# Kernel tuning notes

Measured on AMD Instinct MI355X. Metric: run time of the kernel, lower is better.

Reference implementation:

```python
import jax, jax.numpy as jnp
import numpy as np
import math

D_MODEL = 512
NHEAD = 8
HEAD = D_MODEL // NHEAD


def _pe(length, d):
    pos = np.arange(length)[:, None].astype(np.float32)
    div = np.exp(np.arange(0, d, 2).astype(np.float32) * (-math.log(10000.0) / d))
    pe = np.zeros((length, d), np.float32)
    pe[:, 0::2] = np.sin(pos * div)
    pe[:, 1::2] = np.cos(pos * div)
    return jnp.asarray(pe)


def _ln(x, g, b, eps=1e-5):
    m = x.mean(-1, keepdims=True)
    v = ((x - m) ** 2).mean(-1, keepdims=True)
    return (x - m) / jnp.sqrt(v + eps) * g + b


def _mha(q_in, k_in, v_in, w_in, b_in, w_out, b_out, mask=None):
    d = q_in.shape[-1]
    wq, wk, wv = jnp.split(w_in, 3, axis=0)
    bq, bk, bv = jnp.split(b_in, 3, axis=0)
    B, Sq, _ = q_in.shape
    Sk = k_in.shape[1]
    q = (q_in @ wq.T + bq).reshape(B, Sq, NHEAD, HEAD)
    k = (k_in @ wk.T + bk).reshape(B, Sk, NHEAD, HEAD)
    v = (v_in @ wv.T + bv).reshape(B, Sk, NHEAD, HEAD)
    s = jnp.einsum('bqhd,bkhd->bhqk', q, k) / math.sqrt(HEAD)
    if mask is not None:
        s = s + mask
    a = jax.nn.softmax(s, axis=-1)
    o = jnp.einsum('bhqk,bkhd->bqhd', a, v).reshape(B, Sq, d)
    return o @ w_out.T + b_out


def setup_inputs() -> dict:
    rng = np.random.default_rng(0)
    def r(*s):
        return jnp.asarray(rng.standard_normal(s, dtype=np.float32) * 0.02)
    L, d, ff, di, do = 6, 512, 2048, 64, 64
    B, S, T = 4, 512, 256
    return dict(
        src=jnp.asarray(rng.standard_normal((B, S, di), dtype=np.float32)),
        tgt=jnp.asarray(rng.standard_normal((B, T, do), dtype=np.float32)),
        enc_in_w=r(d, di), enc_in_b=r(d),
        dec_in_w=r(d, do), dec_in_b=r(d),
        out_w=r(do, d), out_b=r(do),
        enc_attn_w=r(L, 3 * d, d), enc_attn_b=r(L, 3 * d),
        enc_out_w=r(L, d, d), enc_out_b=r(L, d),
        enc_ff1_w=r(L, ff, d), enc_ff1_b=r(L, ff),
        enc_ff2_w=r(L, d, ff), enc_ff2_b=r(L, d),
        enc_ln1_g=jnp.ones((L, d)), enc_ln1_b=jnp.zeros((L, d)),
        enc_ln2_g=jnp.ones((L, d)), enc_ln2_b=jnp.zeros((L, d)),
        dec_sa_w=r(L, 3 * d, d), dec_sa_b=r(L, 3 * d),
        dec_sa_out_w=r(L, d, d), dec_sa_out_b=r(L, d),
        dec_ca_w=r(L, 3 * d, d), dec_ca_b=r(L, 3 * d),
        dec_ca_out_w=r(L, d, d), dec_ca_out_b=r(L, d),
        dec_ff1_w=r(L, ff, d), dec_ff1_b=r(L, ff),
        dec_ff2_w=r(L, d, ff), dec_ff2_b=r(L, d),
        dec_ln1_g=jnp.ones((L, d)), dec_ln1_b=jnp.zeros((L, d)),
        dec_ln2_g=jnp.ones((L, d)), dec_ln2_b=jnp.zeros((L, d)),
        dec_ln3_g=jnp.ones((L, d)), dec_ln3_b=jnp.zeros((L, d)),
    )


def reference(src, tgt, enc_in_w, enc_in_b, dec_in_w, dec_in_b, out_w, out_b,
              enc_attn_w, enc_attn_b, enc_out_w, enc_out_b,
              enc_ff1_w, enc_ff1_b, enc_ff2_w, enc_ff2_b,
              enc_ln1_g, enc_ln1_b, enc_ln2_g, enc_ln2_b,
              dec_sa_w, dec_sa_b, dec_sa_out_w, dec_sa_out_b,
              dec_ca_w, dec_ca_b, dec_ca_out_w, dec_ca_out_b,
              dec_ff1_w, dec_ff1_b, dec_ff2_w, dec_ff2_b,
              dec_ln1_g, dec_ln1_b, dec_ln2_g, dec_ln2_b, dec_ln3_g, dec_ln3_b):
    d = D_MODEL
    sq = math.sqrt(d)
    S, T = src.shape[1], tgt.shape[1]
    L = enc_attn_w.shape[0]
    # encoder: 'cosine' pos encoding (dropout disabled / eval)
    x = (src @ enc_in_w.T + enc_in_b) * sq + _pe(S, d)[None]
    for i in range(L):
        a = _mha(x, x, x, enc_attn_w[i], enc_attn_b[i], enc_out_w[i], enc_out_b[i])
        x = _ln(x + a, enc_ln1_g[i], enc_ln1_b[i])
        f = jax.nn.relu(x @ enc_ff1_w[i].T + enc_ff1_b[i]) @ enc_ff2_w[i].T + enc_ff2_b[i]
        x = _ln(x + f, enc_ln2_g[i], enc_ln2_b[i])
    memory = x
    # decoder: teacher-forced prefix loop == single causal-masked pass.
    # NOTE: original adds pe[0] to EVERY step (pos_encoder on a length-1 slice).
    y = (tgt @ dec_in_w.T + dec_in_b) * sq + _pe(1, d)[0]
    mask = jnp.where(jnp.tril(jnp.ones((T, T), bool)), 0.0, -1e9).astype(y.dtype)
    for i in range(L):
        a = _mha(y, y, y, dec_sa_w[i], dec_sa_b[i], dec_sa_out_w[i], dec_sa_out_b[i], mask)
        y = _ln(y + a, dec_ln1_g[i], dec_ln1_b[i])
        c = _mha(y, memory, memory, dec_ca_w[i], dec_ca_b[i], dec_ca_out_w[i], dec_ca_out_b[i])
        y = _ln(y + c, dec_ln2_g[i], dec_ln2_b[i])
        f = jax.nn.relu(y @ dec_ff1_w[i].T + dec_ff1_b[i]) @ dec_ff2_w[i].T + dec_ff2_b[i]
        y = _ln(y + f, dec_ln3_g[i], dec_ln3_b[i])
    return y @ out_w.T + out_b
```

## Files before the change

kernel.cpp:

```cpp
#include <hip/hip_runtime.h>
#include <hip/hip_bf16.h>
#include <math.h>

#define BB 4
#define SEQ 512
#define TGT 256
#define DM 512
#define FFD 2048
#define NH 8
#define HD 64
#define NL 6

typedef unsigned short u16;
typedef __attribute__((ext_vector_type(4))) float f4;
typedef __attribute__((ext_vector_type(4))) unsigned short us4;
typedef __attribute__((ext_vector_type(8))) unsigned short us8;
typedef __attribute__((ext_vector_type(8))) short s8;

__device__ inline u16 f2b(float f) {
    __hip_bfloat16 h = __float2bfloat16(f);
    return *reinterpret_cast<u16*>(&h);
}
__device__ inline float b2f(u16 u) {
    unsigned int x = ((unsigned int)u) << 16;
    float f;
    __builtin_memcpy(&f, &x, 4);
    return f;
}
__device__ inline us4 cvt4(f4 v) {
    us4 u;
    u.x = f2b(v.x); u.y = f2b(v.y); u.z = f2b(v.z); u.w = f2b(v.w);
    return u;
}

__global__ __launch_bounds__(256) void cast4_k(const float* __restrict__ in,
                                               u16* __restrict__ out, int n4)
{
    int i = blockIdx.x * blockDim.x + threadIdx.x;
    if (i < n4) ((us4*)out)[i] = cvt4(((const f4*)in)[i]);
}

template <int RELU, int OUTF32, int BM>
__global__ __launch_bounds__(256) void mgemm_k(
    const u16* __restrict__ A, const u16* __restrict__ W,
    const float* __restrict__ bias, const u16* __restrict__ resid,
    void* __restrict__ Cv, int M, int N, int K, float alpha)
{
    constexpr int MI = BM / 32;
    __shared__ u16 As[2][BM][72];
    __shared__ u16 Bs[2][64][72];
    const int bm = blockIdx.y * BM, bn = blockIdx.x * 64;
    const int tid = threadIdx.x;
    const int wave = tid >> 6, lane = tid & 63;
    const int wr = (wave >> 1) * (BM / 2), wc = (wave & 1) * 32;
    const int lm = lane & 15, quad = lane >> 4;
    const int sbr = tid >> 2, sbc = (tid & 3) * 16;
    const int sar = (BM == 64) ? (tid >> 2) : (tid >> 3);
    const int sac = (BM == 64) ? ((tid & 3) * 16) : ((tid & 7) * 8);

    const u16* Arow = A + (size_t)(bm + sar) * K + sac;
    const u16* Wrow = W + (size_t)(bn + sbr) * K + sbc;

    us8 a0 = *(const us8*)(Arow);
    us8 a1;
    if (BM == 64) a1 = *(const us8*)(Arow + 8);
    us8 b0 = *(const us8*)(Wrow);
    us8 b1 = *(const us8*)(Wrow + 8);

    f4 acc[MI][2];
#pragma unroll
    for (int i = 0; i < MI; i++)
#pragma unroll
        for (int j = 0; j < 2; j++) acc[i][j] = (f4)(0.f);

    const int nk = K >> 6;
    *(us8*)&As[0][sar][sac] = a0;
    if (BM == 64) *(us8*)&As[0][sar][sac + 8] = a1;
    *(us8*)&Bs[0][sbr][sbc] = b0;
    *(us8*)&Bs[0][sbr][sbc + 8] = b1;
    __syncthreads();

    for (int t = 0; t < nk; t++) {
        const int cb = t & 1;
        if (t + 1 < nk) {
            int off = (t + 1) << 6;
            a0 = *(const us8*)(Arow + off);
            if (BM == 64) a1 = *(const us8*)(Arow + off + 8);
            b0 = *(const us8*)(Wrow + off);
            b1 = *(const us8*)(Wrow + off + 8);
        }
#pragma unroll
        for (int ks = 0; ks < 2; ks++) {
            s8 af[MI], bfr[2];
#pragma unroll
            for (int i = 0; i < MI; i++) af[i] = *(const s8*)&As[cb][wr + i * 16 + lm][ks * 32 + quad * 8];
#pragma unroll
            for (int j = 0; j < 2; j++) bfr[j] = *(const s8*)&Bs[cb][wc + j * 16 + lm][ks * 32 + quad * 8];
#pragma unroll
            for (int i = 0; i < MI; i++)
#pragma unroll
                for (int j = 0; j < 2; j++)
                    acc[i][j] = __builtin_amdgcn_mfma_f32_16x16x32_bf16(af[i], bfr[j], acc[i][j], 0, 0, 0);
        }
        if (t + 1 < nk) {
            const int nb = cb ^ 1;
            *(us8*)&As[nb][sar][sac] = a0;
            if (BM == 64) *(us8*)&As[nb][sar][sac + 8] = a1;
            *(us8*)&Bs[nb][sbr][sbc] = b0;
            *(us8*)&Bs[nb][sbr][sbc + 8] = b1;
            __syncthreads();
        }
    }

#pragma unroll
    for (int j = 0; j < 2; j++) {
        int n = bn + wc + j * 16 + lm;
        float bv = bias[n];
#pragma unroll
        for (int i = 0; i < MI; i++) {
#pragma unroll
            for (int r = 0; r < 4; r++) {
                int m = bm + wr + i * 16 + quad * 4 + r;
                float v = (acc[i][j][r] + bv) * alpha;
                if (RELU) v = fmaxf(v, 0.f);
                size_t off = (size_t)m * N + n;
                if (resid) v += b2f(resid[off]);
                if (OUTF32) ((float*)Cv)[off] = v;
                else        ((u16*)Cv)[off]  = f2b(v);
            }
        }
    }
}

template <int CAUSAL>
__global__ __launch_bounds__(256) void flash_k(
    const u16* __restrict__ Q, int qs,
    const u16* __restrict__ Kp, int ks,
    const u16* __restrict__ V, int vs,
    u16* __restrict__ O, int Sq, int Sk)
{
    __shared__ u16 Qs[64][72];
    __shared__ u16 Ks[128][72];
    __shared__ u16 Vs[64][136];
    __shared__ u16 Ps[4][16][136];
    const int bm = blockIdx.x * 64;
    const int bh = blockIdx.y, b = bh >> 3, h = bh & 7;
    const int tid = threadIdx.x;
    const int wave = tid >> 6, lane = tid & 63;
    const int lm = lane & 15, quad = lane >> 4;

    const u16* Qb = Q + (size_t)(b * Sq + bm) * qs + h * HD;
    {
        int r = tid >> 2, c = (tid & 3) * 16;
        *(us8*)&Qs[r][c]     = *(const us8*)(Qb + (size_t)r * qs + c);
        *(us8*)&Qs[r][c + 8] = *(const us8*)(Qb + (size_t)r * qs + c + 8);
    }

    float mrow[4], lrow[4];
    f4 o[4];
#pragma unroll
    for (int r = 0; r < 4; r++) { mrow[r] = -1e30f; lrow[r] = 0.f; }
#pragma unroll
    for (int nt = 0; nt < 4; nt++) o[nt] = (f4)(0.f);

    const u16* Kb = Kp + (size_t)(b * Sk) * ks + h * HD;
    const u16* Vb = V + (size_t)(b * Sk) * vs + h * HD;
    int nkt = Sk >> 7;
    if (CAUSAL) { int lim = (bm + 63) / 128 + 1; if (lim < nkt) nkt = lim; }

    const int vd = tid & 63, vkb = tid >> 6;
    const int kr = tid >> 3, kc8 = (tid & 7) * 8;

    for (int kt = 0; kt < nkt; kt++) {
        const u16* Kt = Kb + ((size_t)kt << 7) * ks;
        const u16* Vt = Vb + ((size_t)kt << 7) * vs;
#pragma unroll
        for (int p = 0; p < 4; p++) {
            int r = p * 32 + kr;
            *(us8*)&Ks[r][kc8] = *(const us8*)(Kt + (size_t)r * ks + kc8);
        }
#pragma unroll
        for (int p = 0; p < 32; p++) {
            int kv = p * 4 + vkb;
            Vs[vd][kv] = Vt[(size_t)kv * vs + vd];
        }
        __syncthreads();

        f4 sa[8];
#pragma unroll
        for (int nt = 0; nt < 8; nt++) sa[nt] = (f4)(0.f);
#pragma unroll
        for (int ks2 = 0; ks2 < 2; ks2++) {
            s8 aq = *(const s8*)&Qs[wave * 16 + lm][ks2 * 32 + quad * 8];
#pragma unroll
            for (int nt = 0; nt < 8; nt++) {
                s8 bk = *(const s8*)&Ks[nt * 16 + lm][ks2 * 32 + quad * 8];
                sa[nt] = __builtin_amdgcn_mfma_f32_16x16x32_bf16(aq, bk, sa[nt], 0, 0, 0);
            }
        }
        float tmx[4] = {-1e30f, -1e30f, -1e30f, -1e30f};
#pragma unroll
        for (int nt = 0; nt < 8; nt++) {
#pragma unroll
            for (int r = 0; r < 4; r++) {
                float v = sa[nt][r] * 0.125f;
                if (CAUSAL) {
                    int col = (kt << 7) + nt * 16 + lm;
                    int row = bm + wave * 16 + quad * 4 + r;
                    if (col > row) v = -1e30f;
                }
                sa[nt][r] = v;
                tmx[r] = fmaxf(tmx[r], v);
            }
        }
#pragma unroll
        for (int st = 1; st < 16; st <<= 1)
#pragma unroll
            for (int r = 0; r < 4; r++) tmx[r] = fmaxf(tmx[r], __shfl_xor(tmx[r], st));
        float al[4];
#pragma unroll
        for (int r = 0; r < 4; r++) {
            float mn = fmaxf(mrow[r], tmx[r]);
            al[r] = __expf(mrow[r] - mn);
            mrow[r] = mn;
        }
        float ts[4] = {0.f, 0.f, 0.f, 0.f};
#pragma unroll
        for (int nt = 0; nt < 8; nt++) {
#pragma unroll
            for (int r = 0; r < 4; r++) {
                float pe = __expf(sa[nt][r] - mrow[r]);
                sa[nt][r] = pe;
                ts[r] += pe;
            }
        }
#pragma unroll
        for (int st = 1; st < 16; st <<= 1)
#pragma unroll
            for (int r = 0; r < 4; r++) ts[r] += __shfl_xor(ts[r], st);
#pragma unroll
        for (int r = 0; r < 4; r++) lrow[r] = lrow[r] * al[r] + ts[r];
#pragma unroll
        for (int nt = 0; nt < 4; nt++)
#pragma unroll
            for (int r = 0; r < 4; r++) o[nt][r] *= al[r];
#pragma unroll
        for (int nt = 0; nt < 8; nt++)
#pragma unroll
            for (int r = 0; r < 4; r++)
                Ps[wave][quad * 4 + r][nt * 16 + lm] = f2b(sa[nt][r]);
#pragma unroll
        for (int kc = 0; kc < 4; kc++) {
            s8 ap = *(const s8*)&Ps[wave][lm][kc * 32 + quad * 8];
#pragma unroll
            for (int nt = 0; nt < 4; nt++) {
                s8 bv = *(const s8*)&Vs[nt * 16 + lm][kc * 32 + quad * 8];
                o[nt] = __builtin_amdgcn_mfma_f32_16x16x32_bf16(ap, bv, o[nt], 0, 0, 0);
            }
        }
        __syncthreads();
    }

    float inv[4];
#pragma unroll
    for (int r = 0; r < 4; r++) inv[r] = 1.f / lrow[r];
#pragma unroll
    for (int nt = 0; nt < 4; nt++) {
#pragma unroll
        for (int r = 0; r < 4; r++) {
            int m = bm + wave * 16 + quad * 4 + r;
            O[(size_t)(b * Sq + m) * DM + h * HD + nt * 16 + lm] = f2b(o[nt][r] * inv[r]);
        }
    }
}

__global__ void add_pe_enc(u16* __restrict__ x)
{
    int idx = blockIdx.x * blockDim.x + threadIdx.x;
    if (idx >= BB * SEQ * DM) return;
    int c = idx % DM;
    int s = (idx / DM) % SEQ;
    float dv = expf((float)(c & ~1) * (-9.210340371976184f / (float)DM));
    float ang = (float)s * dv;
    x[idx] = f2b(b2f(x[idx]) + ((c & 1) ? cosf(ang) : sinf(ang)));
}

__global__ void add_pe_dec(u16* __restrict__ x, int n)
{
    int idx = blockIdx.x * blockDim.x + threadIdx.x;
    if (idx >= n) return;
    if (idx & 1) x[idx] = f2b(b2f(x[idx]) + 1.f);
}

__global__ __launch_bounds__(256) void ln_k(u16* __restrict__ x,
                                            const float* __restrict__ g,
                                            const float* __restrict__ b)
{
    int row = blockIdx.x;
    u16* xr = x + (size_t)row * DM;
    int tid = threadIdx.x;
    float v0 = b2f(xr[tid]), v1 = b2f(xr[tid + 256]);
    __shared__ float red[256];
    red[tid] = v0 + v1;
    __syncthreads();
    for (int st = 128; st > 0; st >>= 1) {
        if (tid < st) red[tid] += red[tid + st];
        __syncthreads();
    }
    float mean = red[0] * (1.f / DM);
    __syncthreads();
    float d0 = v0 - mean, d1 = v1 - mean;
    red[tid] = d0 * d0 + d1 * d1;
    __syncthreads();
    for (int st = 128; st > 0; st >>= 1) {
        if (tid < st) red[tid] += red[tid + st];
        __syncthreads();
    }
    float rstd = rsqrtf(red[0] * (1.f / DM) + 1e-5f);
    xr[tid]       = f2b(d0 * rstd * g[tid]       + b[tid]);
    xr[tid + 256] = f2b(d1 * rstd * g[tid + 256] + b[tid + 256]);
}

static inline dim3 mg64(int M, int N) { return dim3(N / 64, M / 64); }
static inline dim3 mg32(int M, int N) { return dim3(N / 64, M / 32); }
static inline void cast_t(const float* in, u16* out, size_t n, hipStream_t s) {
    int n4 = (int)(n / 4);
    cast4_k<<<(n4 + 255) / 256, 256, 0, s>>>(in, out, n4);
}

extern "C" void kernel_launch(void* const* d_in, const int* in_sizes, int n_in,
                              void* d_out, int out_size, void* d_ws, size_t ws_size,
                              hipStream_t stream)
{
    const float* src       = (const float*)d_in[0];
    const float* tgt       = (const float*)d_in[1];
    const float* enc_in_w  = (const float*)d_in[2];
    const float* enc_in_b  = (const float*)d_in[3];
    const float* dec_in_w  = (const float*)d_in[4];
    const float* dec_in_b  = (const float*)d_in[5];
    const float* out_w     = (const float*)d_in[6];
    const float* out_b     = (const float*)d_in[7];
    const float* enc_attn_w = (const float*)d_in[8];
    const float* enc_attn_b = (const float*)d_in[9];
    const float* enc_out_w  = (const float*)d_in[10];
    const float* enc_out_b  = (const float*)d_in[11];
    const float* enc_ff1_w  = (const float*)d_in[12];
    const float* enc_ff1_b  = (const float*)d_in[13];
    const float* enc_ff2_w  = (const float*)d_in[14];
    const float* enc_ff2_b  = (const float*)d_in[15];
    const float* enc_ln1_g  = (const float*)d_in[16];
    const float* enc_ln1_b  = (const float*)d_in[17];
    const float* enc_ln2_g  = (const float*)d_in[18];
    const float* enc_ln2_b  = (const float*)d_in[19];
    const float* dec_sa_w     = (const float*)d_in[20];
    const float* dec_sa_b     = (const float*)d_in[21];
    const float* dec_sa_out_w = (const float*)d_in[22];
    const float* dec_sa_out_b = (const float*)d_in[23];
    const float* dec_ca_w     = (const float*)d_in[24];
    const float* dec_ca_b     = (const float*)d_in[25];
    const float* dec_ca_out_w = (const float*)d_in[26];
    const float* dec_ca_out_b = (const float*)d_in[27];
    const float* dec_ff1_w    = (const float*)d_in[28];
    const float* dec_ff1_b    = (const float*)d_in[29];
    const float* dec_ff2_w    = (const float*)d_in[30];
    const float* dec_ff2_b    = (const float*)d_in[31];
    const float* dec_ln1_g    = (const float*)d_in[32];
    const float* dec_ln1_b    = (const float*)d_in[33];
    const float* dec_ln2_g    = (const float*)d_in[34];
    const float* dec_ln2_b    = (const float*)d_in[35];
    const float* dec_ln3_g    = (const float*)d_in[36];
    const float* dec_ln3_b    = (const float*)d_in[37];

    u16* p = (u16*)d_ws;
    u16* xa   = p; p += (size_t)BB * SEQ * DM;
    u16* xb   = p; p += (size_t)BB * SEQ * DM;
    u16* reg1 = p; p += (size_t)BB * SEQ * FFD;
    u16* tbuf = p; p += (size_t)BB * SEQ * DM;
    u16* ya   = p; p += (size_t)BB * TGT * DM;
    u16* yb   = p; p += (size_t)BB * TGT * DM;
    u16* wb   = p;

    const float SQD = 22.627416997969522f;
    const int ME = BB * SEQ;
    const int MD = BB * TGT;
    const int BH = BB * NH;

    const size_t SZ_ATTN = (size_t)NL * 3 * DM * DM;
    const size_t SZ_OUT  = (size_t)NL * DM * DM;
    const size_t SZ_FF1  = (size_t)NL * FFD * DM;
    const size_t SZ_FF2  = (size_t)NL * DM * FFD;

    u16* q = wb;
    u16* src_b     = q; q += (size_t)BB * SEQ * HD;
    u16* enc_in_wb = q; q += (size_t)DM * HD;
    u16* enc_at_wb = q; q += SZ_ATTN;
    u16* enc_ow_wb = q; q += SZ_OUT;
    u16* enc_f1_wb = q; q += SZ_FF1;
    u16* enc_f2_wb = q; q += SZ_FF2;
    cast_t(src,        src_b,     (size_t)BB * SEQ * HD, stream);
    cast_t(enc_in_w,   enc_in_wb, (size_t)DM * HD,       stream);
    cast_t(enc_attn_w, enc_at_wb, SZ_ATTN,               stream);
    cast_t(enc_out_w,  enc_ow_wb, SZ_OUT,                stream);
    cast_t(enc_ff1_w,  enc_f1_wb, SZ_FF1,                stream);
    cast_t(enc_ff2_w,  enc_f2_wb, SZ_FF2,                stream);

    mgemm_k<0, 0, 64><<<mg64(ME, DM), 256, 0, stream>>>(src_b, enc_in_wb, enc_in_b, nullptr, xa, ME, DM, HD, SQD);
    add_pe_enc<<<(ME * DM + 255) / 256, 256, 0, stream>>>(xa);

    u16* cur = xa; u16* alt = xb;
    for (int i = 0; i < NL; i++) {
        const u16* W = enc_at_wb + (size_t)i * 3 * DM * DM;
        const float* Bw = enc_attn_b + (size_t)i * 3 * DM;
        mgemm_k<0, 0, 64><<<mg64(ME, 3 * DM), 256, 0, stream>>>(cur, W, Bw, nullptr, reg1, ME, 3 * DM, DM, 1.f);
        flash_k<0><<<dim3(SEQ / 64, BH), 256, 0, stream>>>(reg1, 3 * DM, reg1 + DM, 3 * DM, reg1 + 2 * DM, 3 * DM, tbuf, SEQ, SEQ);
        mgemm_k<0, 0, 32><<<mg32(ME, DM), 256, 0, stream>>>(tbuf, enc_ow_wb + (size_t)i * DM * DM, enc_out_b + (size_t)i * DM, cur, alt, ME, DM, DM, 1.f);
        ln_k<<<ME, 256, 0, stream>>>(alt, enc_ln1_g + (size_t)i * DM, enc_ln1_b + (size_t)i * DM);
        { u16* t = cur; cur = alt; alt = t; }
        mgemm_k<1, 0, 64><<<mg64(ME, FFD), 256, 0, stream>>>(cur, enc_f1_wb + (size_t)i * FFD * DM, enc_ff1_b + (size_t)i * FFD, nullptr, reg1, ME, FFD, DM, 1.f);
        mgemm_k<0, 0, 32><<<mg32(ME, DM), 256, 0, stream>>>(reg1, enc_f2_wb + (size_t)i * DM * FFD, enc_ff2_b + (size_t)i * DM, cur, alt, ME, DM, FFD, 1.f);
        ln_k<<<ME, 256, 0, stream>>>(alt, enc_ln2_g + (size_t)i * DM, enc_ln2_b + (size_t)i * DM);
        { u16* t = cur; cur = alt; alt = t; }
    }
    u16* mem = cur;

    q = wb;
    u16* tgt_b       = q; q += (size_t)BB * TGT * HD;
    u16* dec_in_wb   = q; q += (size_t)DM * HD;
    u16* out_wb      = q; q += (size_t)HD * DM;
    u16* dec_sa_wb   = q; q += SZ_ATTN;
    u16* dec_sao_wb  = q; q += SZ_OUT;
    u16* dec_ca_wb   = q; q += SZ_ATTN;
    u16* dec_cao_wb  = q; q += SZ_OUT;
    u16* dec_f1_wb   = q; q += SZ_FF1;
    u16* dec_f2_wb   = q; q += SZ_FF2;
    cast_t(tgt,          tgt_b,      (size_t)BB * TGT * HD, stream);
    cast_t(dec_in_w,     dec_in_wb,  (size_t)DM * HD,       stream);
    cast_t(out_w,        out_wb,     (size_t)HD * DM,       stream);
    cast_t(dec_sa_w,     dec_sa_wb,  SZ_ATTN,               stream);
    cast_t(dec_sa_out_w, dec_sao_wb, SZ_OUT,                stream);
    cast_t(dec_ca_w,     dec_ca_wb,  SZ_ATTN,               stream);
    cast_t(dec_ca_out_w, dec_cao_wb, SZ_OUT,                stream);
    cast_t(dec_ff1_w,    dec_f1_wb,  SZ_FF1,                stream);
    cast_t(dec_ff2_w,    dec_f2_wb,  SZ_FF2,                stream);

    mgemm_k<0, 0, 32><<<mg32(MD, DM), 256, 0, stream>>>(tgt_b, dec_in_wb, dec_in_b, nullptr, ya, MD, DM, HD, SQD);
    add_pe_dec<<<(MD * DM + 255) / 256, 256, 0, stream>>>(ya, MD * DM);

    u16* dc = ya; u16* da = yb;
    for (int i = 0; i < NL; i++) {
        const u16* W = dec_sa_wb + (size_t)i * 3 * DM * DM;
        const float* Bw = dec_sa_b + (size_t)i * 3 * DM;
        mgemm_k<0, 0, 64><<<mg64(MD, 3 * DM), 256, 0, stream>>>(dc, W, Bw, nullptr, reg1, MD, 3 * DM, DM, 1.f);
        flash_k<1><<<dim3(TGT / 64, BH), 256, 0, stream>>>(reg1, 3 * DM, reg1 + DM, 3 * DM, reg1 + 2 * DM, 3 * DM, tbuf, TGT, TGT);
        mgemm_k<0, 0, 32><<<mg32(MD, DM), 256, 0, stream>>>(tbuf, dec_sao_wb + (size_t)i * DM * DM, dec_sa_out_b + (size_t)i * DM, dc, da, MD, DM, DM, 1.f);
        ln_k<<<MD, 256, 0, stream>>>(da, dec_ln1_g + (size_t)i * DM, dec_ln1_b + (size_t)i * DM);
        { u16* t = dc; dc = da; da = t; }

        const u16* Wc = dec_ca_wb + (size_t)i * 3 * DM * DM;
        const float* Bc = dec_ca_b + (size_t)i * 3 * DM;
        u16* qbuf = reg1;
        u16* kvp  = reg1 + (size_t)MD * DM;
        mgemm_k<0, 0, 32><<<mg32(MD, DM), 256, 0, stream>>>(dc, Wc, Bc, nullptr, qbuf, MD, DM, DM, 1.f);
        mgemm_k<0, 0, 64><<<mg64(ME, 2 * DM), 256, 0, stream>>>(mem, Wc + (size_t)DM * DM, Bc + DM, nullptr, kvp, ME, 2 * DM, DM, 1.f);
        flash_k<0><<<dim3(TGT / 64, BH), 256, 0, stream>>>(qbuf, DM, kvp, 2 * DM, kvp + DM, 2 * DM, tbuf, TGT, SEQ);
        mgemm_k<0, 0, 32><<<mg32(MD, DM), 256, 0, stream>>>(tbuf, dec_cao_wb + (size_t)i * DM * DM, dec_ca_out_b + (size_t)i * DM, dc, da, MD, DM, DM, 1.f);
        ln_k<<<MD, 256, 0, stream>>>(da, dec_ln2_g + (size_t)i * DM, dec_ln2_b + (size_t)i * DM);
        { u16* t = dc; dc = da; da = t; }

        mgemm_k<1, 0, 64><<<mg64(MD, FFD), 256, 0, stream>>>(dc, dec_f1_wb + (size_t)i * FFD * DM, dec_ff1_b + (size_t)i * FFD, nullptr, reg1, MD, FFD, DM, 1.f);
        mgemm_k<0, 0, 32><<<mg32(MD, DM), 256, 0, stream>>>(reg1, dec_f2_wb + (size_t)i * DM * FFD, dec_ff2_b + (size_t)i * DM, dc, da, MD, DM, FFD, 1.f);
        ln_k<<<MD, 256, 0, stream>>>(da, dec_ln3_g + (size_t)i * DM, dec_ln3_b + (size_t)i * DM);
        { u16* t = dc; dc = da; da = t; }
    }

    mgemm_k<0, 1, 32><<<mg32(MD, HD), 256, 0, stream>>>(dc, out_wb, out_b, nullptr, (float*)d_out, MD, HD, DM, 1.f);
}
```

Measured before the change: 1.318 ms.

## Batch weight casts, fuse PE into GEMM epilogue, hoist cross-attn KV projection

Replaces the fifteen separate fp32-to-bf16 cast launches with a single segmented cast kernel. The positional-encoding adds are folded into the input-projection GEMM epilogues. The six per-layer cross-attention K/V projections of encoder memory become one wide GEMM, using a stacked weight copy and a gathered bias. This cuts kernel launch overhead and extra elementwise passes and gives one larger GEMM with better occupancy, at the cost of more workspace and an extra weight copy in the cast pass.

```diff
diff --git a/kernel.cpp b/kernel.cpp
--- a/kernel.cpp
+++ b/kernel.cpp
@@ -33,14 +33,32 @@
     return u;
 }
 
-__global__ __launch_bounds__(256) void cast4_k(const float* __restrict__ in,
-                                               u16* __restrict__ out, int n4)
+struct CastSegs {
+    const float* src[24];
+    u16* dst[24];
+    int cum[25];
+    int nseg;
+};
+
+__global__ __launch_bounds__(256) void castseg_k(CastSegs cs)
 {
     int i = blockIdx.x * blockDim.x + threadIdx.x;
-    if (i < n4) ((us4*)out)[i] = cvt4(((const f4*)in)[i]);
-}
-
-template <int RELU, int OUTF32, int BM>
+    if (i >= cs.cum[cs.nseg]) return;
+    int s = 0;
+    while (i >= cs.cum[s + 1]) s++;
+    int local = i - cs.cum[s];
+    ((us4*)cs.dst[s])[local] = cvt4(((const f4*)cs.src[s])[local]);
+}
+
+__global__ void kvbias_k(const float* __restrict__ dec_ca_b, float* __restrict__ out)
+{
+    int idx = blockIdx.x * blockDim.x + threadIdx.x;
+    if (idx >= NL * 2 * DM) return;
+    int layer = idx >> 10, j = idx & 1023;
+    out[idx] = dec_ca_b[layer * 3 * DM + DM + j];
+}
+
+template <int RELU, int OUTF32, int BM, int PE>
 __global__ __launch_bounds__(256) void mgemm_k(
     const u16* __restrict__ A, const u16* __restrict__ W,
     const float* __restrict__ bias, const u16* __restrict__ resid,
@@ -116,12 +134,19 @@
     for (int j = 0; j < 2; j++) {
         int n = bn + wc + j * 16 + lm;
         float bv = bias[n];
+        float dv = 0.f;
+        if (PE == 1) dv = expf((float)(n & ~1) * (-9.210340371976184f / (float)DM));
 #pragma unroll
         for (int i = 0; i < MI; i++) {
 #pragma unroll
             for (int r = 0; r < 4; r++) {
                 int m = bm + wr + i * 16 + quad * 4 + r;
                 float v = (acc[i][j][r] + bv) * alpha;
+                if (PE == 1) {
+                    float ang = (float)(m & (SEQ - 1)) * dv;
+                    v += (n & 1) ? cosf(ang) : sinf(ang);
+                }
+                if (PE == 2) { if (n & 1) v += 1.f; }
                 if (RELU) v = fmaxf(v, 0.f);
                 size_t off = (size_t)m * N + n;
                 if (resid) v += b2f(resid[off]);
@@ -274,24 +299,6 @@
     }
 }
 
-__global__ void add_pe_enc(u16* __restrict__ x)
-{
-    int idx = blockIdx.x * blockDim.x + threadIdx.x;
-    if (idx >= BB * SEQ * DM) return;
-    int c = idx % DM;
-    int s = (idx / DM) % SEQ;
-    float dv = expf((float)(c & ~1) * (-9.210340371976184f / (float)DM));
-    float ang = (float)s * dv;
-    x[idx] = f2b(b2f(x[idx]) + ((c & 1) ? cosf(ang) : sinf(ang)));
-}
-
-__global__ void add_pe_dec(u16* __restrict__ x, int n)
-{
-    int idx = blockIdx.x * blockDim.x + threadIdx.x;
-    if (idx >= n) return;
-    if (idx & 1) x[idx] = f2b(b2f(x[idx]) + 1.f);
-}
-
 __global__ __launch_bounds__(256) void ln_k(u16* __restrict__ x,
                                             const float* __restrict__ g,
                                             const float* __restrict__ b)
@@ -323,10 +330,6 @@
 
 static inline dim3 mg64(int M, int N) { return dim3(N / 64, M / 64); }
 static inline dim3 mg32(int M, int N) { return dim3(N / 64, M / 32); }
-static inline void cast_t(const float* in, u16* out, size_t n, hipStream_t s) {
-    int n4 = (int)(n / 4);
-    cast4_k<<<(n4 + 255) / 256, 256, 0, s>>>(in, out, n4);
-}
 
 extern "C" void kernel_launch(void* const* d_in, const int* in_sizes, int n_in,
                               void* d_out, int out_size, void* d_ws, size_t ws_size,
@@ -371,107 +374,119 @@
     const float* dec_ln3_g    = (const float*)d_in[36];
     const float* dec_ln3_b    = (const float*)d_in[37];
 
-    u16* p = (u16*)d_ws;
-    u16* xa   = p; p += (size_t)BB * SEQ * DM;
-    u16* xb   = p; p += (size_t)BB * SEQ * DM;
-    u16* reg1 = p; p += (size_t)BB * SEQ * FFD;
-    u16* tbuf = p; p += (size_t)BB * SEQ * DM;
-    u16* ya   = p; p += (size_t)BB * TGT * DM;
-    u16* yb   = p; p += (size_t)BB * TGT * DM;
-    u16* wb   = p;
-
-    const float SQD = 22.627416997969522f;
     const int ME = BB * SEQ;
     const int MD = BB * TGT;
     const int BH = BB * NH;
+    const float SQD = 22.627416997969522f;
 
     const size_t SZ_ATTN = (size_t)NL * 3 * DM * DM;
     const size_t SZ_OUT  = (size_t)NL * DM * DM;
-    const size_t SZ_FF1  = (size_t)NL * FFD * DM;
-    const size_t SZ_FF2  = (size_t)NL * DM * FFD;
-
-    u16* q = wb;
-    u16* src_b     = q; q += (size_t)BB * SEQ * HD;
-    u16* enc_in_wb = q; q += (size_t)DM * HD;
-    u16* enc_at_wb = q; q += SZ_ATTN;
-    u16* enc_ow_wb = q; q += SZ_OUT;
-    u16* enc_f1_wb = q; q += SZ_FF1;
-    u16* enc_f2_wb = q; q += SZ_FF2;
-    cast_t(src,        src_b,     (size_t)BB * SEQ * HD, stream);
-    cast_t(enc_in_w,   enc_in_wb, (size_t)DM * HD,       stream);
-    cast_t(enc_attn_w, enc_at_wb, SZ_ATTN,               stream);
-    cast_t(enc_out_w,  enc_ow_wb, SZ_OUT,                stream);
-    cast_t(enc_ff1_w,  enc_f1_wb, SZ_FF1,                stream);
-    cast_t(enc_ff2_w,  enc_f2_wb, SZ_FF2,                stream);
-
-    mgemm_k<0, 0, 64><<<mg64(ME, DM), 256, 0, stream>>>(src_b, enc_in_wb, enc_in_b, nullptr, xa, ME, DM, HD, SQD);
-    add_pe_enc<<<(ME * DM + 255) / 256, 256, 0, stream>>>(xa);
+    const size_t SZ_FF   = (size_t)NL * FFD * DM;
+
+    float* fp = (float*)d_ws;
+    float* kvbias = fp; fp += NL * 2 * DM;
+    u16* p = (u16*)fp;
+    u16* xa   = p; p += (size_t)ME * DM;
+    u16* xb   = p; p += (size_t)ME * DM;
+    u16* reg1 = p; p += (size_t)ME * FFD;
+    u16* tbuf = p; p += (size_t)ME * DM;
+    u16* ya   = p; p += (size_t)MD * DM;
+    u16* yb   = p; p += (size_t)MD * DM;
+    u16* kvall = p; p += (size_t)ME * NL * 2 * DM;
+    u16* src_b     = p; p += (size_t)ME * HD;
+    u16* tgt_b     = p; p += (size_t)MD * HD;
+    u16* enc_in_wb = p; p += (size_t)DM * HD;
+    u16* dec_in_wb = p; p += (size_t)DM * HD;
+    u16* out_wb    = p; p += (size_t)HD * DM;
+    u16* enc_at_wb = p; p += SZ_ATTN;
+    u16* enc_ow_wb = p; p += SZ_OUT;
+    u16* enc_f1_wb = p; p += SZ_FF;
+    u16* enc_f2_wb = p; p += SZ_FF;
+    u16* dec_sa_wb = p; p += SZ_ATTN;
+    u16* dec_sao_wb = p; p += SZ_OUT;
+    u16* dec_ca_wb = p; p += SZ_ATTN;
+    u16* dec_cao_wb = p; p += SZ_OUT;
+    u16* dec_f1_wb = p; p += SZ_FF;
+    u16* dec_f2_wb = p; p += SZ_FF;
+    u16* kvstack   = p; p += (size_t)NL * 2 * DM * DM;
+
+    CastSegs cs;
+    int ns = 0;
+    auto seg = [&](const float* s, u16* d, size_t n) {
+        cs.src[ns] = s; cs.dst[ns] = d;
+        cs.cum[ns + 1] = cs.cum[ns] + (int)(n / 4);
+        ns++;
+    };
+    cs.cum[0] = 0;
+    seg(src,          src_b,     (size_t)ME * HD);
+    seg(tgt,          tgt_b,     (size_t)MD * HD);
+    seg(enc_in_w,     enc_in_wb, (size_t)DM * HD);
+    seg(dec_in_w,     dec_in_wb, (size_t)DM * HD);
+    seg(out_w,        out_wb,    (size_t)HD * DM);
+    seg(enc_attn_w,   enc_at_wb, SZ_ATTN);
+    seg(enc_out_w,    enc_ow_wb, SZ_OUT);
+    seg(enc_ff1_w,    enc_f1_wb, SZ_FF);
+    seg(enc_ff2_w,    enc_f2_wb, SZ_FF);
+    seg(dec_sa_w,     dec_sa_wb, SZ_ATTN);
+    seg(dec_sa_out_w, dec_sao_wb, SZ_OUT);
+    seg(dec_ca_w,     dec_ca_wb, SZ_ATTN);
+    seg(dec_ca_out_w, dec_cao_wb, SZ_OUT);
+    seg(dec_ff1_w,    dec_f1_wb, SZ_FF);
+    seg(dec_ff2_w,    dec_f2_wb, SZ_FF);
+    for (int i = 0; i < NL; i++)
+        seg(dec_ca_w + (size_t)i * 3 * DM * DM + (size_t)DM * DM,
+            kvstack + (size_t)i * 2 * DM * DM, (size_t)2 * DM * DM);
+    cs.nseg = ns;
+    castseg_k<<<(cs.cum[ns] + 255) / 256, 256, 0, stream>>>(cs);
+    kvbias_k<<<(NL * 2 * DM + 255) / 256, 256, 0, stream>>>(dec_ca_b, kvbias);
+
+    mgemm_k<0, 0, 64, 1><<<mg64(ME, DM), 256, 0, stream>>>(src_b, enc_in_wb, enc_in_b, nullptr, xa, ME, DM, HD, SQD);
 
     u16* cur = xa; u16* alt = xb;
     for (int i = 0; i < NL; i++) {
         const u16* W = enc_at_wb + (size_t)i * 3 * DM * DM;
         const float* Bw = enc_attn_b + (size_t)i * 3 * DM;
-        mgemm_k<0, 0, 64><<<mg64(ME, 3 * DM), 256, 0, stream>>>(cur, W, Bw, nullptr, reg1, ME, 3 * DM, DM, 1.f);
+        mgemm_k<0, 0, 64, 0><<<mg64(ME, 3 * DM), 256, 0, stream>>>(cur, W, Bw, nullptr, reg1, ME, 3 * DM, DM, 1.f);
         flash_k<0><<<dim3(SEQ / 64, BH), 256, 0, stream>>>(reg1, 3 * DM, reg1 + DM, 3 * DM, reg1 + 2 * DM, 3 * DM, tbuf, SEQ, SEQ);
-        mgemm_k<0, 0, 32><<<mg32(ME, DM), 256, 0, stream>>>(tbuf, enc_ow_wb + (size_t)i * DM * DM, enc_out_b + (size_t)i * DM, cur, alt, ME, DM, DM, 1.f);
+        mgemm_k<0, 0, 32, 0><<<mg32(ME, DM), 256, 0, stream>>>(tbuf, enc_ow_wb + (size_t)i * DM * DM, enc_out_b + (size_t)i * DM, cur, alt, ME, DM, DM, 1.f);
         ln_k<<<ME, 256, 0, stream>>>(alt, enc_ln1_g + (size_t)i * DM, enc_ln1_b + (size_t)i * DM);
         { u16* t = cur; cur = alt; alt = t; }
-        mgemm_k<1, 0, 64><<<mg64(ME, FFD), 256, 0, stream>>>(cur, enc_f1_wb + (size_t)i * FFD * DM, enc_ff1_b + (size_t)i * FFD, nullptr, reg1, ME, FFD, DM, 1.f);
-        mgemm_k<0, 0, 32><<<mg32(ME, DM), 256, 0, stream>>>(reg1, enc_f2_wb + (size_t)i * DM * FFD, enc_ff2_b + (size_t)i * DM, cur, alt, ME, DM, FFD, 1.f);
+        mgemm_k<1, 0, 64, 0><<<mg64(ME, FFD), 256, 0, stream>>>(cur, enc_f1_wb + (size_t)i * FFD * DM, enc_ff1_b + (size_t)i * FFD, nullptr, reg1, ME, FFD, DM, 1.f);
+        mgemm_k<0, 0, 32, 0><<<mg32(ME, DM), 256, 0, stream>>>(reg1, enc_f2_wb + (size_t)i * DM * FFD, enc_ff2_b + (size_t)i * DM, cur, alt, ME, DM, FFD, 1.f);
         ln_k<<<ME, 256, 0, stream>>>(alt, enc_ln2_g + (size_t)i * DM, enc_ln2_b + (size_t)i * DM);
         { u16* t = cur; cur = alt; alt = t; }
     }
     u16* mem = cur;
 
-    q = wb;
-    u16* tgt_b       = q; q += (size_t)BB * TGT * HD;
-    u16* dec_in_wb   = q; q += (size_t)DM * HD;
-    u16* out_wb      = q; q += (size_t)HD * DM;
-    u16* dec_sa_wb   = q; q += SZ_ATTN;
-    u16* dec_sao_wb  = q; q += SZ_OUT;
-    u16* dec_ca_wb   = q; q += SZ_ATTN;
-    u16* dec_cao_wb  = q; q += SZ_OUT;
-    u16* dec_f1_wb   = q; q += SZ_FF1;
-    u16* dec_f2_wb   = q; q += SZ_FF2;
-    cast_t(tgt,          tgt_b,      (size_t)BB * TGT * HD, stream);
-    cast_t(dec_in_w,     dec_in_wb,  (size_t)DM * HD,       stream);
-    cast_t(out_w,        out_wb,     (size_t)HD * DM,       stream);
-    cast_t(dec_sa_w,     dec_sa_wb,  SZ_ATTN,               stream);
-    cast_t(dec_sa_out_w, dec_sao_wb, SZ_OUT,                stream);
-    cast_t(dec_ca_w,     dec_ca_wb,  SZ_ATTN,               stream);
-    cast_t(dec_ca_out_w, dec_cao_wb, SZ_OUT,                stream);
-    cast_t(dec_ff1_w,    dec_f1_wb,  SZ_FF1,                stream);
-    cast_t(dec_ff2_w,    dec_f2_wb,  SZ_FF2,                stream);
-
-    mgemm_k<0, 0, 32><<<mg32(MD, DM), 256, 0, stream>>>(tgt_b, dec_in_wb, dec_in_b, nullptr, ya, MD, DM, HD, SQD);
-    add_pe_dec<<<(MD * DM + 255) / 256, 256, 0, stream>>>(ya, MD * DM);
+    mgemm_k<0, 0, 64, 0><<<mg64(ME, NL * 2 * DM), 256, 0, stream>>>(mem, kvstack, kvbias, nullptr, kvall, ME, NL * 2 * DM, DM, 1.f);
+
+    mgemm_k<0, 0, 32, 2><<<mg32(MD, DM), 256, 0, stream>>>(tgt_b, dec_in_wb, dec_in_b, nullptr, ya, MD, DM, HD, SQD);
 
     u16* dc = ya; u16* da = yb;
     for (int i = 0; i < NL; i++) {
         const u16* W = dec_sa_wb + (size_t)i * 3 * DM * DM;
         const float* Bw = dec_sa_b + (size_t)i * 3 * DM;
-        mgemm_k<0, 0, 64><<<mg64(MD, 3 * DM), 256, 0, stream>>>(dc, W, Bw, nullptr, reg1, MD, 3 * DM, DM, 1.f);
+        mgemm_k<0, 0, 64, 0><<<mg64(MD, 3 * DM), 256, 0, stream>>>(dc, W, Bw, nullptr, reg1, MD, 3 * DM, DM, 1.f);
         flash_k<1><<<dim3(TGT / 64, BH), 256, 0, stream>>>(reg1, 3 * DM, reg1 + DM, 3 * DM, reg1 + 2 * DM, 3 * DM, tbuf, TGT, TGT);
-        mgemm_k<0, 0, 32><<<mg32(MD, DM), 256, 0, stream>>>(tbuf, dec_sao_wb + (size_t)i * DM * DM, dec_sa_out_b + (size_t)i * DM, dc, da, MD, DM, DM, 1.f);
+        mgemm_k<0, 0, 32, 0><<<mg32(MD, DM), 256, 0, stream>>>(tbuf, dec_sao_wb + (size_t)i * DM * DM, dec_sa_out_b + (size_t)i * DM, dc, da, MD, DM, DM, 1.f);
         ln_k<<<MD, 256, 0, stream>>>(da, dec_ln1_g + (size_t)i * DM, dec_ln1_b + (size_t)i * DM);
         { u16* t = dc; dc = da; da = t; }
 
         const u16* Wc = dec_ca_wb + (size_t)i * 3 * DM * DM;
         const float* Bc = dec_ca_b + (size_t)i * 3 * DM;
         u16* qbuf = reg1;
-        u16* kvp  = reg1 + (size_t)MD * DM;
-        mgemm_k<0, 0, 32><<<mg32(MD, DM), 256, 0, stream>>>(dc, Wc, Bc, nullptr, qbuf, MD, DM, DM, 1.f);
-        mgemm_k<0, 0, 64><<<mg64(ME, 2 * DM), 256, 0, stream>>>(mem, Wc + (size_t)DM * DM, Bc + DM, nullptr, kvp, ME, 2 * DM, DM, 1.f);
-        flash_k<0><<<dim3(TGT / 64, BH), 256, 0, stream>>>(qbuf, DM, kvp, 2 * DM, kvp + DM, 2 * DM, tbuf, TGT, SEQ);
-        mgemm_k<0, 0, 32><<<mg32(MD, DM), 256, 0, stream>>>(tbuf, dec_cao_wb + (size_t)i * DM * DM, dec_ca_out_b + (size_t)i * DM, dc, da, MD, DM, DM, 1.f);
+        mgemm_k<0, 0, 32, 0><<<mg32(MD, DM), 256, 0, stream>>>(dc, Wc, Bc, nullptr, qbuf, MD, DM, DM, 1.f);
+        const u16* kvl = kvall + (size_t)i * 2 * DM;
+        flash_k<0><<<dim3(TGT / 64, BH), 256, 0, stream>>>(qbuf, DM, kvl, NL * 2 * DM, kvl + DM, NL * 2 * DM, tbuf, TGT, SEQ);
+        mgemm_k<0, 0, 32, 0><<<mg32(MD, DM), 256, 0, stream>>>(tbuf, dec_cao_wb + (size_t)i * DM * DM, dec_ca_out_b + (size_t)i * DM, dc, da, MD, DM, DM, 1.f);
         ln_k<<<MD, 256, 0, stream>>>(da, dec_ln2_g + (size_t)i * DM, dec_ln2_b + (size_t)i * DM);
         { u16* t = dc; dc = da; da = t; }
 
-        mgemm_k<1, 0, 64><<<mg64(MD, FFD), 256, 0, stream>>>(dc, dec_f1_wb + (size_t)i * FFD * DM, dec_ff1_b + (size_t)i * FFD, nullptr, reg1, MD, FFD, DM, 1.f);
-        mgemm_k<0, 0, 32><<<mg32(MD, DM), 256, 0, stream>>>(reg1, dec_f2_wb + (size_t)i * DM * FFD, dec_ff2_b + (size_t)i * DM, dc, da, MD, DM, FFD, 1.f);
+        mgemm_k<1, 0, 64, 0><<<mg64(MD, FFD), 256, 0, stream>>>(dc, dec_f1_wb + (size_t)i * FFD * DM, dec_ff1_b + (size_t)i * FFD, nullptr, reg1, MD, FFD, DM, 1.f);
+        mgemm_k<0, 0, 32, 0><<<mg32(MD, DM), 256, 0, stream>>>(reg1, dec_f2_wb + (size_t)i * DM * FFD, dec_ff2_b + (size_t)i * DM, dc, da, MD, DM, FFD, 1.f);
         ln_k<<<MD, 256, 0, stream>>>(da, dec_ln3_g + (size_t)i * DM, dec_ln3_b + (size_t)i * DM);
         { u16* t = dc; dc = da; da = t; }
     }
 
-    mgemm_k<0, 1, 32><<<mg32(MD, HD), 256, 0, stream>>>(dc, out_wb, out_b, nullptr, (float*)d_out, MD, HD, DM, 1.f);
-}
+    mgemm_k<0, 1, 32, 0><<<mg32(MD, HD), 256, 0, stream>>>(dc, out_wb, out_b, nullptr, (float*)d_out, MD, HD, DM, 1.f);
+}
```

After: 1.276 ms. 1.03x faster.
